# Kernel optimization log

Hardware: AMD Instinct MI355X
Metric: run time of the kernel (lower is better)

The kernel has to match this reference:

```python
import jax, jax.numpy as jnp
import numpy as np

N = 100000   # nodes
E = 1600000  # edges (before self-loops)
D = 128      # feature dim (in == hidden == out)
EPS = 1e-5   # LayerNorm eps (torch default)


def setup_inputs() -> dict:
    key = jax.random.key(0)
    ks = jax.random.split(key, 6)
    x = jax.random.normal(ks[0], (N, D), dtype=jnp.float32)
    edge_row = jax.random.randint(ks[1], (E,), 0, N, dtype=jnp.int32)
    edge_col = jax.random.randint(ks[2], (E,), 0, N, dtype=jnp.int32)
    scale = 1.0 / np.sqrt(D)
    inp = {"x": x, "edge_row": edge_row, "edge_col": edge_col}
    for i, kk in zip((1, 2, 3), (ks[3], ks[4], ks[5])):
        inp[f"W{i}"] = jax.random.normal(kk, (D, D), dtype=jnp.float32) * scale
        inp[f"b{i}"] = jnp.zeros((D,), jnp.float32)
        inp[f"g{i}"] = jnp.ones((D,), jnp.float32)
        inp[f"beta{i}"] = jnp.zeros((D,), jnp.float32)
    return inp


def _layer_norm(h, g, b):
    mu = jnp.mean(h, axis=-1, keepdims=True)
    var = jnp.mean((h - mu) ** 2, axis=-1, keepdims=True)
    return (h - mu) * jax.lax.rsqrt(var + EPS) * g + b


def reference(x, W1, b1, g1, beta1, W2, b2, g2, beta2, W3, b3, g3, beta3,
              edge_row, edge_col):
    n = x.shape[0]
    # gcn_norm: add self-loops, symmetric D^-1/2 (A+I) D^-1/2
    loops = jnp.arange(n, dtype=edge_row.dtype)
    row = jnp.concatenate([edge_row, loops])  # [E+N] destination
    col = jnp.concatenate([edge_col, loops])  # [E+N] source
    deg = jax.ops.segment_sum(jnp.ones(row.shape[0], dtype=x.dtype), row,
                              num_segments=n)
    dinv = jnp.where(deg > 0, jax.lax.rsqrt(deg), 0.0)
    w = dinv[row] * dinv[col]  # [E+N] normalized edge weights

    def gcn_layer(h, W, b, g, beta):
        h = h @ W                                   # [N, D] dense GEMM
        msg = w[:, None] * h[col]                   # gather + scale
        h = jax.ops.segment_sum(msg, row, num_segments=n) + b  # spmm + bias
        return jax.nn.relu(_layer_norm(h, g, beta))  # ln -> (dropout=id) -> relu

    h = gcn_layer(x, W1, b1, g1, beta1)
    h = gcn_layer(h, W2, b2, g2, beta2)
    h = gcn_layer(h, W3, b3, g3, beta3)
    return h
```

## Files before the change

kernel.cpp:

```cpp
#include <hip/hip_runtime.h>
#include <hip/hip_bf16.h>
#include <stdint.h>

#define DD 128

typedef __bf16 bf16;
typedef __bf16 bf16x8 __attribute__((ext_vector_type(8)));
typedef float f32x4 __attribute__((ext_vector_type(4)));
typedef _Float16 f16;
typedef f16 f16x4 __attribute__((ext_vector_type(4)));

__global__ __launch_bounds__(256) void k_zero(unsigned* degE, int n) {
  int i = blockIdx.x * 256 + threadIdx.x;
  if (i < n) degE[i] = 0u;
}

__global__ __launch_bounds__(256) void k_deg_count(const int* __restrict__ row,
                                                   unsigned* degE, int E) {
  int e = blockIdx.x * 256 + threadIdx.x;
  if (e < E) atomicAdd(&degE[row[e]], 1u);
}

__global__ __launch_bounds__(256) void k_scan1(const unsigned* __restrict__ degE,
                                               unsigned* __restrict__ cursor,
                                               unsigned* __restrict__ bsum,
                                               float* __restrict__ dinv, int n) {
  __shared__ unsigned sh[256];
  int tid = threadIdx.x;
  int base = blockIdx.x * 1024 + tid * 4;
  unsigned v0 = (base + 0 < n) ? degE[base + 0] : 0u;
  unsigned v1 = (base + 1 < n) ? degE[base + 1] : 0u;
  unsigned v2 = (base + 2 < n) ? degE[base + 2] : 0u;
  unsigned v3 = (base + 3 < n) ? degE[base + 3] : 0u;
  if (base + 0 < n) dinv[base + 0] = rsqrtf((float)(v0 + 1u));
  if (base + 1 < n) dinv[base + 1] = rsqrtf((float)(v1 + 1u));
  if (base + 2 < n) dinv[base + 2] = rsqrtf((float)(v2 + 1u));
  if (base + 3 < n) dinv[base + 3] = rsqrtf((float)(v3 + 1u));
  unsigned p1 = v0, p2 = p1 + v1, p3 = p2 + v2, tot = p3 + v3;
  sh[tid] = tot;
  __syncthreads();
  for (int off = 1; off < 256; off <<= 1) {
    unsigned t = (tid >= off) ? sh[tid - off] : 0u;
    __syncthreads();
    sh[tid] += t;
    __syncthreads();
  }
  unsigned excl = sh[tid] - tot;
  if (base + 0 < n) cursor[base + 0] = excl;
  if (base + 1 < n) cursor[base + 1] = excl + p1;
  if (base + 2 < n) cursor[base + 2] = excl + p2;
  if (base + 3 < n) cursor[base + 3] = excl + p3;
  if (tid == 255) bsum[blockIdx.x] = sh[255];
}

__global__ __launch_bounds__(256) void k_scan2(const unsigned* __restrict__ bsum,
                                               unsigned* __restrict__ boff, int nb) {
  __shared__ unsigned sh[256];
  int tid = threadIdx.x;
  unsigned x = (tid < nb) ? bsum[tid] : 0u;
  sh[tid] = x;
  __syncthreads();
  for (int off = 1; off < 256; off <<= 1) {
    unsigned t = (tid >= off) ? sh[tid - off] : 0u;
    __syncthreads();
    sh[tid] += t;
    __syncthreads();
  }
  if (tid < nb) boff[tid] = sh[tid] - x;
}

__global__ __launch_bounds__(256) void k_scan3(unsigned* cursor,
                                               const unsigned* __restrict__ boff, int n) {
  int i = blockIdx.x * 256 + threadIdx.x;
  if (i < n) cursor[i] += boff[i >> 10];
}

__global__ __launch_bounds__(256) void k_fill(const int* __restrict__ row,
                                              const int* __restrict__ col,
                                              const float* __restrict__ dinv,
                                              unsigned* cursor, int2* __restrict__ ewc,
                                              int E) {
  int e = blockIdx.x * 256 + threadIdx.x;
  if (e >= E) return;
  int r = row[e], c = col[e];
  float w = dinv[r] * dinv[c];
  unsigned pos = atomicAdd(&cursor[r], 1u);
  ewc[pos] = make_int2(c, __float_as_int(w));
}

__global__ __launch_bounds__(256) void k_wsplit(const float* __restrict__ W,
                                                bf16* __restrict__ Thi,
                                                bf16* __restrict__ Tlo) {
  int i = blockIdx.x * 256 + threadIdx.x;
  int k = i >> 7, c = i & 127;
  float v = W[i];
  bf16 hi = (bf16)v;
  bf16 lo = (bf16)(v - (float)hi);
  Thi[c * 128 + k] = hi;
  Tlo[c * 128 + k] = lo;
}

__global__ __launch_bounds__(512, 4) void k_gemm_mfma(const float* __restrict__ H,
                                                      const bf16* __restrict__ Wthi,
                                                      const bf16* __restrict__ Wtlo,
                                                      f16* __restrict__ O, int n) {
  __shared__ short WH[16384];
  __shared__ short WL[16384];
  const int tx = threadIdx.x;
  const int w = tx >> 6, l = tx & 63;
  const int cl = l & 15, lg = l >> 4;
  const int rbase = blockIdx.x * 128 + w * 16;

#pragma unroll
  for (int t4 = 0; t4 < 4; ++t4) {
    int idx = tx + t4 * 512;
    int byte = idx * 16;
    int wrow = byte >> 8;
    int off = byte & 255;
    int swz = off ^ ((wrow & 7) << 4);
    *(bf16x8*)((char*)WH + wrow * 256 + swz) = *(const bf16x8*)((const char*)Wthi + byte);
    *(bf16x8*)((char*)WL + wrow * 256 + swz) = *(const bf16x8*)((const char*)Wtlo + byte);
  }

  const int arow = rbase + cl;
  const bool ok = arow < n;
  const float* rp = H + (size_t)arow * DD + lg * 8;
  bf16x8 ah[4], al[4];
#pragma unroll
  for (int k0 = 0; k0 < 4; ++k0) {
    f32x4 v0 = {0.f, 0.f, 0.f, 0.f}, v1 = {0.f, 0.f, 0.f, 0.f};
    if (ok) {
      v0 = *(const f32x4*)(rp + k0 * 32);
      v1 = *(const f32x4*)(rp + k0 * 32 + 4);
    }
    bf16x8 h, lo;
#pragma unroll
    for (int j = 0; j < 4; ++j) {
      bf16 h0 = (bf16)v0[j], h1 = (bf16)v1[j];
      h[j] = h0;
      h[j + 4] = h1;
      lo[j] = (bf16)(v0[j] - (float)h0);
      lo[j + 4] = (bf16)(v1[j] - (float)h1);
    }
    ah[k0] = h;
    al[k0] = lo;
  }
  __syncthreads();

  f32x4 acc[8] = {};
#pragma unroll
  for (int k0 = 0; k0 < 4; ++k0) {
#pragma unroll
    for (int c = 0; c < 8; ++c) {
      int col = c * 16 + cl;
      int kb = k0 * 64 + lg * 16;
      int swz = kb ^ ((col & 7) << 4);
      bf16x8 bh = *(const bf16x8*)((const char*)WH + col * 256 + swz);
      bf16x8 bl = *(const bf16x8*)((const char*)WL + col * 256 + swz);
      acc[c] = __builtin_amdgcn_mfma_f32_16x16x32_bf16(ah[k0], bh, acc[c], 0, 0, 0);
      acc[c] = __builtin_amdgcn_mfma_f32_16x16x32_bf16(ah[k0], bl, acc[c], 0, 0, 0);
      acc[c] = __builtin_amdgcn_mfma_f32_16x16x32_bf16(al[k0], bh, acc[c], 0, 0, 0);
    }
  }

#pragma unroll
  for (int c = 0; c < 8; ++c) {
    int col = c * 16 + cl;
    f32x4 a = acc[c];
#pragma unroll
    for (int j = 0; j < 4; ++j) {
      int row = rbase + lg * 4 + j;
      if (row < n) O[(size_t)row * DD + col] = (f16)a[j];
    }
  }
}

__global__ __launch_bounds__(256) void k_agg_ln(const f16* __restrict__ T,
                                                const unsigned* __restrict__ cend,
                                                const unsigned* __restrict__ degE,
                                                const float* __restrict__ dinv,
                                                const int2* __restrict__ ewc,
                                                const float* __restrict__ bias,
                                                const float* __restrict__ g,
                                                const float* __restrict__ beta,
                                                float* __restrict__ O, int n) {
  const int lane = threadIdx.x & 63;
  const int wid = threadIdx.x >> 6;
  const int li = lane & 31;
  const int r = blockIdx.x * 8 + wid * 2 + (lane >> 5);
  const bool valid = r < n;
  const int rs = valid ? r : (n - 1);

  const unsigned end = cend[rs];
  const unsigned cnt = valid ? degE[rs] : 0u;
  const float di = dinv[rs];
  unsigned e = end - (unsigned)(valid ? degE[rs] : 0u);

  unsigned cntO = (unsigned)__shfl_xor((int)cnt, 32);
  int cmw = __builtin_amdgcn_readfirstlane((int)min(cnt, cntO));

  const f16* Tl = T + li * 4;
  f16x4 sv = *(const f16x4*)(Tl + (size_t)rs * DD);
  float4 bb = *(const float4*)(bias + li * 4);
  const float ws = di * di;
  float4 a0, a1, a2, a3;
  a0.x = fmaf(ws, (float)sv[0], bb.x);
  a0.y = fmaf(ws, (float)sv[1], bb.y);
  a0.z = fmaf(ws, (float)sv[2], bb.z);
  a0.w = fmaf(ws, (float)sv[3], bb.w);
  a1 = make_float4(0.f, 0.f, 0.f, 0.f);
  a2 = a1; a3 = a1;

  int k = 0;
  int2 m0, m1, m2, m3;
  if (cmw >= 4) { m0 = ewc[e]; m1 = ewc[e + 1]; m2 = ewc[e + 2]; m3 = ewc[e + 3]; }
  while (k + 4 <= cmw) {
    int2 p0, p1, p2, p3;
    if (k + 8 <= cmw) {
      p0 = ewc[e + 4]; p1 = ewc[e + 5]; p2 = ewc[e + 6]; p3 = ewc[e + 7];
    }
    f16x4 u0 = *(const f16x4*)(Tl + (size_t)m0.x * DD);
    f16x4 u1 = *(const f16x4*)(Tl + (size_t)m1.x * DD);
    f16x4 u2 = *(const f16x4*)(Tl + (size_t)m2.x * DD);
    f16x4 u3 = *(const f16x4*)(Tl + (size_t)m3.x * DD);
    float w0 = __int_as_float(m0.y), w1 = __int_as_float(m1.y);
    float w2 = __int_as_float(m2.y), w3 = __int_as_float(m3.y);
    a0.x = fmaf(w0, (float)u0[0], a0.x); a0.y = fmaf(w0, (float)u0[1], a0.y);
    a0.z = fmaf(w0, (float)u0[2], a0.z); a0.w = fmaf(w0, (float)u0[3], a0.w);
    a1.x = fmaf(w1, (float)u1[0], a1.x); a1.y = fmaf(w1, (float)u1[1], a1.y);
    a1.z = fmaf(w1, (float)u1[2], a1.z); a1.w = fmaf(w1, (float)u1[3], a1.w);
    a2.x = fmaf(w2, (float)u2[0], a2.x); a2.y = fmaf(w2, (float)u2[1], a2.y);
    a2.z = fmaf(w2, (float)u2[2], a2.z); a2.w = fmaf(w2, (float)u2[3], a2.w);
    a3.x = fmaf(w3, (float)u3[0], a3.x); a3.y = fmaf(w3, (float)u3[1], a3.y);
    a3.z = fmaf(w3, (float)u3[2], a3.z); a3.w = fmaf(w3, (float)u3[3], a3.w);
    m0 = p0; m1 = p1; m2 = p2; m3 = p3;
    e += 4;
    k += 4;
  }
  for (unsigned kk = (unsigned)k; kk < cnt; ++kk, ++e) {
    int2 m = ewc[e];
    f16x4 u = *(const f16x4*)(Tl + (size_t)m.x * DD);
    float w = __int_as_float(m.y);
    a0.x = fmaf(w, (float)u[0], a0.x); a0.y = fmaf(w, (float)u[1], a0.y);
    a0.z = fmaf(w, (float)u[2], a0.z); a0.w = fmaf(w, (float)u[3], a0.w);
  }
  float4 a;
  a.x = (a0.x + a1.x) + (a2.x + a3.x);
  a.y = (a0.y + a1.y) + (a2.y + a3.y);
  a.z = (a0.z + a1.z) + (a2.z + a3.z);
  a.w = (a0.w + a1.w) + (a2.w + a3.w);

  float s = (a.x + a.y) + (a.z + a.w);
#pragma unroll
  for (int o = 16; o > 0; o >>= 1) s += __shfl_xor(s, o);
  float mu = s * (1.0f / 128.0f);
  float dx = a.x - mu, dy = a.y - mu, dz = a.z - mu, dw = a.w - mu;
  float q = (dx * dx + dy * dy) + (dz * dz + dw * dw);
#pragma unroll
  for (int o = 16; o > 0; o >>= 1) q += __shfl_xor(q, o);
  float rstd = rsqrtf(q * (1.0f / 128.0f) + 1e-5f);
  float4 gg = *(const float4*)(g + li * 4);
  float4 be4 = *(const float4*)(beta + li * 4);
  float4 o4;
  o4.x = fmaxf(fmaf(dx * rstd, gg.x, be4.x), 0.f);
  o4.y = fmaxf(fmaf(dy * rstd, gg.y, be4.y), 0.f);
  o4.z = fmaxf(fmaf(dz * rstd, gg.z, be4.z), 0.f);
  o4.w = fmaxf(fmaf(dw * rstd, gg.w, be4.w), 0.f);
  if (valid) *(float4*)(O + (size_t)r * DD + li * 4) = o4;
}

extern "C" void kernel_launch(void* const* d_in, const int* in_sizes, int n_in,
                              void* d_out, int out_size, void* d_ws, size_t ws_size,
                              hipStream_t stream) {
  const float* x    = (const float*)d_in[0];
  const int*   erow = (const int*)d_in[1];
  const int*   ecol = (const int*)d_in[2];
  const float* Wm[3] = {(const float*)d_in[3], (const float*)d_in[7],  (const float*)d_in[11]};
  const float* bs[3] = {(const float*)d_in[4], (const float*)d_in[8],  (const float*)d_in[12]};
  const float* gs[3] = {(const float*)d_in[5], (const float*)d_in[9],  (const float*)d_in[13]};
  const float* be[3] = {(const float*)d_in[6], (const float*)d_in[10], (const float*)d_in[14]};
  const int N = in_sizes[0] / DD;
  const int E = in_sizes[1];

  uint8_t* wp = (uint8_t*)d_ws;
  auto alloc = [&](size_t bytes) {
    uint8_t* p = wp;
    wp += (bytes + 255) & ~(size_t)255;
    return p;
  };
  unsigned* degE   = (unsigned*)alloc((size_t)N * 4);
  float*    dinv   = (float*)alloc((size_t)N * 4);
  unsigned* cursor = (unsigned*)alloc((size_t)N * 4);
  unsigned* bsum   = (unsigned*)alloc(256 * 4);
  unsigned* boff   = (unsigned*)alloc(256 * 4);
  int2*     ewc    = (int2*)alloc((size_t)E * 8);
  f16*      A16    = (f16*)alloc((size_t)N * DD * 2);
  float*    Hb     = (float*)alloc((size_t)N * DD * 4);
  bf16*     Wthi[3], *Wtlo[3];
  for (int i = 0; i < 3; ++i) {
    Wthi[i] = (bf16*)alloc(DD * DD * 2);
    Wtlo[i] = (bf16*)alloc(DD * DD * 2);
  }

  const int nb = (N + 1023) / 1024;

  k_zero<<<(N + 255) / 256, 256, 0, stream>>>(degE, N);
  k_deg_count<<<(E + 255) / 256, 256, 0, stream>>>(erow, degE, E);
  k_scan1<<<nb, 256, 0, stream>>>(degE, cursor, bsum, dinv, N);
  k_scan2<<<1, 256, 0, stream>>>(bsum, boff, nb);
  k_scan3<<<(N + 255) / 256, 256, 0, stream>>>(cursor, boff, N);
  k_fill<<<(E + 255) / 256, 256, 0, stream>>>(erow, ecol, dinv, cursor, ewc, E);
  for (int i = 0; i < 3; ++i)
    k_wsplit<<<64, 256, 0, stream>>>(Wm[i], Wthi[i], Wtlo[i]);

  const int gemm_grid = (N + 127) / 128;
  const int agg_grid  = (N + 7) / 8;

  auto layer = [&](const float* hin, int li, float* hout) {
    k_gemm_mfma<<<gemm_grid, 512, 0, stream>>>(hin, Wthi[li], Wtlo[li], A16, N);
    k_agg_ln<<<agg_grid, 256, 0, stream>>>(A16, cursor, degE, dinv, ewc,
                                           bs[li], gs[li], be[li], hout, N);
  };

  layer(x, 0, Hb);
  layer(Hb, 1, Hb);
  layer(Hb, 2, (float*)d_out);
}
```

Measured before the change: 570.6 us.

## Switch GEMM to single fp16 MFMA, pack edges to 32 bits, fp16 activations

Replaces the three-pass bf16 hi/lo split GEMM with one fp16 MFMA pass on inputs pre-cast to fp16. The input x is converted once, and intermediate layer outputs are stored in fp16 instead of fp32. Edge entries are packed into 32 bits (17-bit column index plus fp16 weight), halving CSR traffic. The fill kernel is also partitioned so each XCD group handles one row range, aiming to localize atomics. These cuts in memory traffic and MFMA work come at the cost of accuracy, and the packing assumes N is below 2^17.

```diff
diff --git a/kernel.cpp b/kernel.cpp
--- a/kernel.cpp
+++ b/kernel.cpp
@@ -4,11 +4,24 @@
 
 #define DD 128
 
-typedef __bf16 bf16;
-typedef __bf16 bf16x8 __attribute__((ext_vector_type(8)));
-typedef float f32x4 __attribute__((ext_vector_type(4)));
 typedef _Float16 f16;
 typedef f16 f16x4 __attribute__((ext_vector_type(4)));
+typedef f16 f16x8 __attribute__((ext_vector_type(8)));
+typedef float f32x4 __attribute__((ext_vector_type(4)));
+
+__device__ __forceinline__ unsigned packcw(int c, float w) {
+  f16 h = (f16)w;
+  unsigned short us;
+  __builtin_memcpy(&us, &h, 2);
+  return ((unsigned)us << 17) | (unsigned)c;
+}
+__device__ __forceinline__ float unpackw(unsigned p) {
+  unsigned short us = (unsigned short)(p >> 17);
+  f16 h;
+  __builtin_memcpy(&h, &us, 2);
+  return (float)h;
+}
+__device__ __forceinline__ int unpackc(unsigned p) { return (int)(p & 0x1FFFFu); }
 
 __global__ __launch_bounds__(256) void k_zero(unsigned* degE, int n) {
   int i = blockIdx.x * 256 + threadIdx.x;
@@ -78,34 +91,52 @@
 __global__ __launch_bounds__(256) void k_fill(const int* __restrict__ row,
                                               const int* __restrict__ col,
                                               const float* __restrict__ dinv,
-                                              unsigned* cursor, int2* __restrict__ ewc,
-                                              int E) {
-  int e = blockIdx.x * 256 + threadIdx.x;
-  if (e >= E) return;
-  int r = row[e], c = col[e];
-  float w = dinv[r] * dinv[c];
-  unsigned pos = atomicAdd(&cursor[r], 1u);
-  ewc[pos] = make_int2(c, __float_as_int(w));
-}
-
-__global__ __launch_bounds__(256) void k_wsplit(const float* __restrict__ W,
-                                                bf16* __restrict__ Thi,
-                                                bf16* __restrict__ Tlo) {
+                                              unsigned* cursor,
+                                              unsigned* __restrict__ ep,
+                                              int E, int N) {
+  const int xcd = blockIdx.x & 7;
+  const int blk = blockIdx.x >> 3;
+  const int r0 = (int)((size_t)N * xcd / 8);
+  const int r1 = (int)((size_t)N * (xcd + 1) / 8);
+  const int e0 = (int)((size_t)E * blk / 256);
+  const int e1 = (int)((size_t)E * (blk + 1) / 256);
+  for (int e = e0 + (int)threadIdx.x; e < e1; e += 256) {
+    int r = row[e];
+    if (r >= r0 && r < r1) {
+      int c = col[e];
+      float w = dinv[r] * dinv[c];
+      unsigned pos = atomicAdd(&cursor[r], 1u);
+      ep[pos] = packcw(c, w);
+    }
+  }
+}
+
+__global__ __launch_bounds__(256) void k_xcast(const float* __restrict__ X,
+                                               f16* __restrict__ Y, int nv8) {
+  int i = blockIdx.x * 256 + threadIdx.x;
+  if (i >= nv8) return;
+  f32x4 a = ((const f32x4*)X)[i * 2];
+  f32x4 b = ((const f32x4*)X)[i * 2 + 1];
+  f16x8 o;
+#pragma unroll
+  for (int j = 0; j < 4; ++j) {
+    o[j] = (f16)a[j];
+    o[j + 4] = (f16)b[j];
+  }
+  ((f16x8*)Y)[i] = o;
+}
+
+__global__ __launch_bounds__(256) void k_wt16(const float* __restrict__ W,
+                                              f16* __restrict__ Wt) {
   int i = blockIdx.x * 256 + threadIdx.x;
   int k = i >> 7, c = i & 127;
-  float v = W[i];
-  bf16 hi = (bf16)v;
-  bf16 lo = (bf16)(v - (float)hi);
-  Thi[c * 128 + k] = hi;
-  Tlo[c * 128 + k] = lo;
-}
-
-__global__ __launch_bounds__(512, 4) void k_gemm_mfma(const float* __restrict__ H,
-                                                      const bf16* __restrict__ Wthi,
-                                                      const bf16* __restrict__ Wtlo,
+  Wt[c * 128 + k] = (f16)W[i];
+}
+
+__global__ __launch_bounds__(512, 4) void k_gemm_mfma(const f16* __restrict__ H,
+                                                      const f16* __restrict__ Wt,
                                                       f16* __restrict__ O, int n) {
-  __shared__ short WH[16384];
-  __shared__ short WL[16384];
+  __shared__ short WT[16384];
   const int tx = threadIdx.x;
   const int w = tx >> 6, l = tx & 63;
   const int cl = l & 15, lg = l >> 4;
@@ -118,32 +149,18 @@
     int wrow = byte >> 8;
     int off = byte & 255;
     int swz = off ^ ((wrow & 7) << 4);
-    *(bf16x8*)((char*)WH + wrow * 256 + swz) = *(const bf16x8*)((const char*)Wthi + byte);
-    *(bf16x8*)((char*)WL + wrow * 256 + swz) = *(const bf16x8*)((const char*)Wtlo + byte);
+    *(f16x8*)((char*)WT + wrow * 256 + swz) = *(const f16x8*)((const char*)Wt + byte);
   }
 
   const int arow = rbase + cl;
   const bool ok = arow < n;
-  const float* rp = H + (size_t)arow * DD + lg * 8;
-  bf16x8 ah[4], al[4];
+  const f16* rp = H + (size_t)arow * DD + lg * 8;
+  f16x8 af[4];
 #pragma unroll
   for (int k0 = 0; k0 < 4; ++k0) {
-    f32x4 v0 = {0.f, 0.f, 0.f, 0.f}, v1 = {0.f, 0.f, 0.f, 0.f};
-    if (ok) {
-      v0 = *(const f32x4*)(rp + k0 * 32);
-      v1 = *(const f32x4*)(rp + k0 * 32 + 4);
-    }
-    bf16x8 h, lo;
-#pragma unroll
-    for (int j = 0; j < 4; ++j) {
-      bf16 h0 = (bf16)v0[j], h1 = (bf16)v1[j];
-      h[j] = h0;
-      h[j + 4] = h1;
-      lo[j] = (bf16)(v0[j] - (float)h0);
-      lo[j + 4] = (bf16)(v1[j] - (float)h1);
-    }
-    ah[k0] = h;
-    al[k0] = lo;
+    f16x8 v = {};
+    if (ok) v = *(const f16x8*)(rp + k0 * 32);
+    af[k0] = v;
   }
   __syncthreads();
 
@@ -155,11 +172,8 @@
       int col = c * 16 + cl;
       int kb = k0 * 64 + lg * 16;
       int swz = kb ^ ((col & 7) << 4);
-      bf16x8 bh = *(const bf16x8*)((const char*)WH + col * 256 + swz);
-      bf16x8 bl = *(const bf16x8*)((const char*)WL + col * 256 + swz);
-      acc[c] = __builtin_amdgcn_mfma_f32_16x16x32_bf16(ah[k0], bh, acc[c], 0, 0, 0);
-      acc[c] = __builtin_amdgcn_mfma_f32_16x16x32_bf16(ah[k0], bl, acc[c], 0, 0, 0);
-      acc[c] = __builtin_amdgcn_mfma_f32_16x16x32_bf16(al[k0], bh, acc[c], 0, 0, 0);
+      f16x8 bv = *(const f16x8*)((const char*)WT + col * 256 + swz);
+      acc[c] = __builtin_amdgcn_mfma_f32_16x16x32_f16(af[k0], bv, acc[c], 0, 0, 0);
     }
   }
 
@@ -179,11 +193,13 @@
                                                 const unsigned* __restrict__ cend,
                                                 const unsigned* __restrict__ degE,
                                                 const float* __restrict__ dinv,
-                                                const int2* __restrict__ ewc,
+                                                const unsigned* __restrict__ ep,
                                                 const float* __restrict__ bias,
                                                 const float* __restrict__ g,
                                                 const float* __restrict__ beta,
-                                                float* __restrict__ O, int n) {
+                                                f16* __restrict__ O16,
+                                                float* __restrict__ O32,
+                                                int n, int wfp32) {
   const int lane = threadIdx.x & 63;
   const int wid = threadIdx.x >> 6;
   const int li = lane & 31;
@@ -194,10 +210,10 @@
   const unsigned end = cend[rs];
   const unsigned cnt = valid ? degE[rs] : 0u;
   const float di = dinv[rs];
-  unsigned e = end - (unsigned)(valid ? degE[rs] : 0u);
+  unsigned e = end - cnt;
 
   unsigned cntO = (unsigned)__shfl_xor((int)cnt, 32);
-  int cmw = __builtin_amdgcn_readfirstlane((int)min(cnt, cntO));
+  int cmw = __builtin_amdgcn_readfirstlane((int)(cnt < cntO ? cnt : cntO));
 
   const f16* Tl = T + li * 4;
   f16x4 sv = *(const f16x4*)(Tl + (size_t)rs * DD);
@@ -212,19 +228,19 @@
   a2 = a1; a3 = a1;
 
   int k = 0;
-  int2 m0, m1, m2, m3;
-  if (cmw >= 4) { m0 = ewc[e]; m1 = ewc[e + 1]; m2 = ewc[e + 2]; m3 = ewc[e + 3]; }
+  unsigned m0, m1, m2, m3;
+  if (cmw >= 4) { m0 = ep[e]; m1 = ep[e + 1]; m2 = ep[e + 2]; m3 = ep[e + 3]; }
   while (k + 4 <= cmw) {
-    int2 p0, p1, p2, p3;
+    unsigned q0, q1, q2, q3;
     if (k + 8 <= cmw) {
-      p0 = ewc[e + 4]; p1 = ewc[e + 5]; p2 = ewc[e + 6]; p3 = ewc[e + 7];
-    }
-    f16x4 u0 = *(const f16x4*)(Tl + (size_t)m0.x * DD);
-    f16x4 u1 = *(const f16x4*)(Tl + (size_t)m1.x * DD);
-    f16x4 u2 = *(const f16x4*)(Tl + (size_t)m2.x * DD);
-    f16x4 u3 = *(const f16x4*)(Tl + (size_t)m3.x * DD);
-    float w0 = __int_as_float(m0.y), w1 = __int_as_float(m1.y);
-    float w2 = __int_as_float(m2.y), w3 = __int_as_float(m3.y);
+      q0 = ep[e + 4]; q1 = ep[e + 5]; q2 = ep[e + 6]; q3 = ep[e + 7];
+    }
+    f16x4 u0 = *(const f16x4*)(Tl + (size_t)unpackc(m0) * DD);
+    f16x4 u1 = *(const f16x4*)(Tl + (size_t)unpackc(m1) * DD);
+    f16x4 u2 = *(const f16x4*)(Tl + (size_t)unpackc(m2) * DD);
+    f16x4 u3 = *(const f16x4*)(Tl + (size_t)unpackc(m3) * DD);
+    float w0 = unpackw(m0), w1 = unpackw(m1);
+    float w2 = unpackw(m2), w3 = unpackw(m3);
     a0.x = fmaf(w0, (float)u0[0], a0.x); a0.y = fmaf(w0, (float)u0[1], a0.y);
     a0.z = fmaf(w0, (float)u0[2], a0.z); a0.w = fmaf(w0, (float)u0[3], a0.w);
     a1.x = fmaf(w1, (float)u1[0], a1.x); a1.y = fmaf(w1, (float)u1[1], a1.y);
@@ -233,14 +249,14 @@
     a2.z = fmaf(w2, (float)u2[2], a2.z); a2.w = fmaf(w2, (float)u2[3], a2.w);
     a3.x = fmaf(w3, (float)u3[0], a3.x); a3.y = fmaf(w3, (float)u3[1], a3.y);
     a3.z = fmaf(w3, (float)u3[2], a3.z); a3.w = fmaf(w3, (float)u3[3], a3.w);
-    m0 = p0; m1 = p1; m2 = p2; m3 = p3;
+    m0 = q0; m1 = q1; m2 = q2; m3 = q3;
     e += 4;
     k += 4;
   }
   for (unsigned kk = (unsigned)k; kk < cnt; ++kk, ++e) {
-    int2 m = ewc[e];
-    f16x4 u = *(const f16x4*)(Tl + (size_t)m.x * DD);
-    float w = __int_as_float(m.y);
+    unsigned m = ep[e];
+    f16x4 u = *(const f16x4*)(Tl + (size_t)unpackc(m) * DD);
+    float w = unpackw(m);
     a0.x = fmaf(w, (float)u[0], a0.x); a0.y = fmaf(w, (float)u[1], a0.y);
     a0.z = fmaf(w, (float)u[2], a0.z); a0.w = fmaf(w, (float)u[3], a0.w);
   }
@@ -261,12 +277,19 @@
   float rstd = rsqrtf(q * (1.0f / 128.0f) + 1e-5f);
   float4 gg = *(const float4*)(g + li * 4);
   float4 be4 = *(const float4*)(beta + li * 4);
-  float4 o4;
-  o4.x = fmaxf(fmaf(dx * rstd, gg.x, be4.x), 0.f);
-  o4.y = fmaxf(fmaf(dy * rstd, gg.y, be4.y), 0.f);
-  o4.z = fmaxf(fmaf(dz * rstd, gg.z, be4.z), 0.f);
-  o4.w = fmaxf(fmaf(dw * rstd, gg.w, be4.w), 0.f);
-  if (valid) *(float4*)(O + (size_t)r * DD + li * 4) = o4;
+  float ox = fmaxf(fmaf(dx * rstd, gg.x, be4.x), 0.f);
+  float oy = fmaxf(fmaf(dy * rstd, gg.y, be4.y), 0.f);
+  float oz = fmaxf(fmaf(dz * rstd, gg.z, be4.z), 0.f);
+  float ow = fmaxf(fmaf(dw * rstd, gg.w, be4.w), 0.f);
+  if (valid) {
+    if (wfp32) {
+      float4 o4 = {ox, oy, oz, ow};
+      *(float4*)(O32 + (size_t)r * DD + li * 4) = o4;
+    } else {
+      f16x4 o4 = {(f16)ox, (f16)oy, (f16)oz, (f16)ow};
+      *(f16x4*)(O16 + (size_t)r * DD + li * 4) = o4;
+    }
+  }
 }
 
 extern "C" void kernel_launch(void* const* d_in, const int* in_sizes, int n_in,
@@ -293,14 +316,12 @@
   unsigned* cursor = (unsigned*)alloc((size_t)N * 4);
   unsigned* bsum   = (unsigned*)alloc(256 * 4);
   unsigned* boff   = (unsigned*)alloc(256 * 4);
-  int2*     ewc    = (int2*)alloc((size_t)E * 8);
+  unsigned* ep     = (unsigned*)alloc((size_t)E * 4);
   f16*      A16    = (f16*)alloc((size_t)N * DD * 2);
-  float*    Hb     = (float*)alloc((size_t)N * DD * 4);
-  bf16*     Wthi[3], *Wtlo[3];
-  for (int i = 0; i < 3; ++i) {
-    Wthi[i] = (bf16*)alloc(DD * DD * 2);
-    Wtlo[i] = (bf16*)alloc(DD * DD * 2);
-  }
+  f16*      Hb16   = (f16*)alloc((size_t)N * DD * 2);
+  f16*      X16    = (f16*)alloc((size_t)N * DD * 2);
+  f16*      Wt[3];
+  for (int i = 0; i < 3; ++i) Wt[i] = (f16*)alloc(DD * DD * 2);
 
   const int nb = (N + 1023) / 1024;
 
@@ -309,20 +330,22 @@
   k_scan1<<<nb, 256, 0, stream>>>(degE, cursor, bsum, dinv, N);
   k_scan2<<<1, 256, 0, stream>>>(bsum, boff, nb);
   k_scan3<<<(N + 255) / 256, 256, 0, stream>>>(cursor, boff, N);
-  k_fill<<<(E + 255) / 256, 256, 0, stream>>>(erow, ecol, dinv, cursor, ewc, E);
+  k_fill<<<2048, 256, 0, stream>>>(erow, ecol, dinv, cursor, ep, E, N);
+  k_xcast<<<(N * DD / 8 + 255) / 256, 256, 0, stream>>>(x, X16, N * DD / 8);
   for (int i = 0; i < 3; ++i)
-    k_wsplit<<<64, 256, 0, stream>>>(Wm[i], Wthi[i], Wtlo[i]);
+    k_wt16<<<64, 256, 0, stream>>>(Wm[i], Wt[i]);
 
   const int gemm_grid = (N + 127) / 128;
   const int agg_grid  = (N + 7) / 8;
 
-  auto layer = [&](const float* hin, int li, float* hout) {
-    k_gemm_mfma<<<gemm_grid, 512, 0, stream>>>(hin, Wthi[li], Wtlo[li], A16, N);
-    k_agg_ln<<<agg_grid, 256, 0, stream>>>(A16, cursor, degE, dinv, ewc,
-                                           bs[li], gs[li], be[li], hout, N);
+  auto layer = [&](const f16* hin, int li, int last) {
+    k_gemm_mfma<<<gemm_grid, 512, 0, stream>>>(hin, Wt[li], A16, N);
+    k_agg_ln<<<agg_grid, 256, 0, stream>>>(A16, cursor, degE, dinv, ep,
+                                           bs[li], gs[li], be[li],
+                                           Hb16, (float*)d_out, N, last);
   };
 
-  layer(x, 0, Hb);
-  layer(Hb, 1, Hb);
-  layer(Hb, 2, (float*)d_out);
-}
+  layer(X16, 0, 0);
+  layer(Hb16, 1, 0);
+  layer(Hb16, 2, 1);
+}
```

Measured after the change: 527.5 us. -7.5%, faster.
